# Kernel optimization log

Hardware: AMD Instinct MI355X
Metric: run time of the kernel (lower is better)

Reference implementation:

```python
import jax, jax.numpy as jnp
import numpy as np

B, N, R, D = 32, 256, 2048, 1024

def setup_inputs() -> dict:
    key = jax.random.key(0)
    ks = jax.random.split(key, 8)
    obj_vecs = jax.random.normal(ks[0], (B, N, D), dtype=jnp.float32)
    attr_vecs = jax.random.normal(ks[1], (B, N, D), dtype=jnp.float32)
    rela_vecs = jax.random.normal(ks[2], (B, R, D), dtype=jnp.float32)
    edges = jax.random.randint(ks[3], (B, R, 2), 0, N, dtype=jnp.int32)
    rela_masks = jnp.ones((B, R, 1), dtype=jnp.float32)
    # learned params: gnn_attr Linear(2D->D), gnn_rela Linear(3D->D)
    W_attr = jax.random.normal(ks[4], (D, 2 * D), dtype=jnp.float32) * 0.02
    b_attr = jnp.zeros((D,), dtype=jnp.float32)
    W_rela = jax.random.normal(ks[5], (D, 3 * D), dtype=jnp.float32) * 0.02
    b_rela = jnp.zeros((D,), dtype=jnp.float32)
    return {"obj_vecs": obj_vecs, "attr_vecs": attr_vecs, "rela_vecs": rela_vecs,
            "edges": edges, "rela_masks": rela_masks,
            "W_attr": W_attr, "b_attr": b_attr, "W_rela": W_rela, "b_rela": b_rela}

def reference(obj_vecs, attr_vecs, rela_vecs, edges, rela_masks,
              W_attr, b_attr, W_rela, b_rela):
    # gnn_attr: Linear(concat[obj,attr]) -> ReLU (-> dropout, identity in eval) + residual
    attr_in = jnp.concatenate([obj_vecs, attr_vecs], axis=-1)          # [B,N,2D]
    new_attr_vecs = jax.nn.relu(jnp.einsum('bnk,dk->bnd', attr_in, W_attr) + b_attr) + attr_vecs
    # gather subject/object node features per edge (per-batch indices)
    subj_idx = edges[:, :, 0:1]                                        # [B,R,1]
    obj_idx = edges[:, :, 1:2]
    subject_vecs = jnp.take_along_axis(obj_vecs, subj_idx, axis=1)     # [B,R,D]
    object_vecs = jnp.take_along_axis(obj_vecs, obj_idx, axis=1)       # [B,R,D]
    # rela_gnn_type == 0: triplet concat [subj | rela | obj]
    triplet = jnp.concatenate([subject_vecs, rela_vecs, object_vecs], axis=-1)  # [B,R,3D]
    new_rela_vecs = jax.nn.relu(jnp.einsum('brk,dk->brd', triplet, W_rela) + b_rela) + rela_vecs
    new_rela_vecs = new_rela_vecs * rela_masks                          # feat_2d_to_3d masking
    return (obj_vecs, new_attr_vecs, new_rela_vecs)
```

## Files before the change

### kernel.cpp

```cpp
#include <hip/hip_runtime.h>
#include <hip/hip_bf16.h>

constexpr int kB = 32;
constexpr int kN = 256;
constexpr int kR = 2048;
constexpr int kD = 1024;

typedef short bf16x8 __attribute__((ext_vector_type(8)));
typedef float f32x4 __attribute__((ext_vector_type(4)));
typedef unsigned short u16x8 __attribute__((ext_vector_type(8)));

__device__ __forceinline__ unsigned short f2bf(float f) {
  union { __hip_bfloat16 h; unsigned short u; } cv;
  cv.h = __float2bfloat16(f);
  return cv.u;
}
__device__ __forceinline__ float bf2f(unsigned short u) {
  union { unsigned int i; float f; } cv;
  cv.i = (unsigned int)u << 16;
  return cv.f;
}

__device__ __forceinline__ void gload_lds16(const void* g, void* l) {
  __builtin_amdgcn_global_load_lds(
      (const __attribute__((address_space(1))) unsigned int*)g,
      (__attribute__((address_space(3))) unsigned int*)l, 16, 0, 0);
}

#define FENCE asm volatile("" ::: "memory")
#define WAITV(n) asm volatile("s_waitcnt vmcnt(" #n ")" ::: "memory")

__global__ void cvt_all(const float* __restrict__ obj,
                        const float* __restrict__ attr,
                        const float* __restrict__ rela,
                        const float* __restrict__ wa,
                        const float* __restrict__ wr,
                        unsigned short* __restrict__ objb,
                        unsigned short* __restrict__ attrb,
                        unsigned short* __restrict__ relab,
                        unsigned short* __restrict__ wab,
                        unsigned short* __restrict__ wrb,
                        float* __restrict__ out0) {
  constexpr long n0 = (long)kB * kN * kD / 8;
  constexpr long c0 = n0;
  constexpr long c1 = c0 + n0;
  constexpr long c2 = c1 + (long)kB * kR * kD / 8;
  constexpr long c3 = c2 + (long)kD * 2 * kD / 8;
  constexpr long c4 = c3 + (long)kD * 3 * kD / 8;
  const long stride = (long)gridDim.x * blockDim.x;
  for (long i = (long)blockIdx.x * blockDim.x + threadIdx.x; i < c4;
       i += stride) {
    const float* s;
    unsigned short* d;
    long j;
    bool isobj = false;
    if (i < c0)      { s = obj;  d = objb;  j = i; isobj = true; }
    else if (i < c1) { s = attr; d = attrb; j = i - c0; }
    else if (i < c2) { s = rela; d = relab; j = i - c1; }
    else if (i < c3) { s = wa;   d = wab;   j = i - c2; }
    else             { s = wr;   d = wrb;   j = i - c3; }
    const float4 a = reinterpret_cast<const float4*>(s)[2 * j];
    const float4 b = reinterpret_cast<const float4*>(s)[2 * j + 1];
    if (isobj) {
      reinterpret_cast<float4*>(out0)[2 * j] = a;
      reinterpret_cast<float4*>(out0)[2 * j + 1] = b;
    }
    u16x8 v;
    v[0] = f2bf(a.x); v[1] = f2bf(a.y); v[2] = f2bf(a.z); v[3] = f2bf(a.w);
    v[4] = f2bf(b.x); v[5] = f2bf(b.y); v[6] = f2bf(b.z); v[7] = f2bf(b.w);
    reinterpret_cast<u16x8*>(d)[j] = v;
  }
}

template <int MODE, int NPANEL>
__device__ __forceinline__ void gemm_body(
    int bid, unsigned short* smem,
    const unsigned short* __restrict__ srcA0,
    const unsigned short* __restrict__ srcA1,
    const unsigned short* __restrict__ Wb, uint32_t koffB,
    const int* __restrict__ edges, const float* __restrict__ masks,
    const unsigned short* __restrict__ residB, const float* __restrict__ bias,
    const unsigned short* __restrict__ P1b,
    const unsigned short* __restrict__ P3b,
    float* __restrict__ outF, unsigned short* __restrict__ outP) {
  constexpr int K_TOT = (MODE == 0) ? 2048 : (MODE == 1) ? 3072 : 1024;
  constexpr int WST = (MODE == 0) ? 2048 : 3072;
  constexpr int T = K_TOT / 64;

  const int x = bid & 7;
  const int col0 = (x >> 1) * 256;
  const int panel = (x & 1) * (NPANEL / 2) + (bid >> 3);
  const int row0 = panel * 256;

  const int tid = threadIdx.x;
  const int w = tid >> 6;
  const int l = tid & 63;

  const int sw = (((l & 3) ^ ((l >> 3) & 3)) << 4);
  const char* pA0[2];
  const char* pA1[2];
  const char* pA2[2];
  const char* pB[2];
#pragma unroll
  for (int r = 0; r < 2; ++r) {
    const int rl = w * 32 + r * 16 + (l >> 2);
    const int m = row0 + rl;
    if constexpr (MODE == 1) {
      const int b = m >> 11;
      const int ri = m & 2047;
      const int2 e =
          *reinterpret_cast<const int2*>(&edges[((size_t)b * kR + ri) * 2]);
      pA0[r] = (const char*)(srcA0 + (size_t)(b * kN + e.x) * kD);
      pA1[r] = (const char*)(srcA1 + (size_t)m * kD);
      pA2[r] = (const char*)(srcA0 + (size_t)(b * kN + e.y) * kD);
    } else {
      pA0[r] = (const char*)(srcA0 + (size_t)m * kD);
      pA1[r] = (MODE == 0) ? (const char*)(srcA1 + (size_t)m * kD) : pA0[r];
      pA2[r] = pA0[r];
    }
    pB[r] = (const char*)Wb + (size_t)(col0 + rl) * WST * 2 + koffB;
  }

  const int wr = w >> 2;
  const int wc = w & 3;
  const int lrow = l & 15;
  const int lgrp = l >> 4;
  const int pgr = ((lgrp ^ ((lrow >> 1) & 3)) << 3);

  f32x4 acc[8][4] = {};
  bf16x8 AfX[4], AfY[4], Bf0[4], Bf1[4];

  auto issueA = [&](int tn, int h, int slot) {
    unsigned short* ra = smem + slot * 32768 + h * 8192;
    const int kb = tn * 64 + h * 32;
#pragma unroll
    for (int r = 0; r < 2; ++r) {
      const char* srcA;
      uint32_t ko;
      if constexpr (MODE == 1) {
        const int seg = kb >> 10;
        srcA = (seg == 1) ? pA1[r] : ((seg == 0) ? pA0[r] : pA2[r]);
        ko = (uint32_t)(kb & 1023) * 2;
      } else if constexpr (MODE == 0) {
        srcA = (kb < 1024) ? pA0[r] : pA1[r];
        ko = (uint32_t)(kb & 1023) * 2;
      } else {
        srcA = pA0[r];
        ko = (uint32_t)kb * 2;
      }
      gload_lds16(srcA + ko + sw, ra + (w * 2 + r) * 512);
    }
  };
  auto issueB = [&](int tn, int h, int slot) {
    unsigned short* rb = smem + slot * 32768 + 16384 + h * 8192;
    const uint32_t kb2 = (uint32_t)(tn * 64 + h * 32) * 2;
#pragma unroll
    for (int r = 0; r < 2; ++r)
      gload_lds16(pB[r] + kb2 + sw, rb + (w * 2 + r) * 512);
  };

#define RD_A4(SET, SLOT, KK, MOFF)                                         \
  _Pragma("unroll")                                                        \
  for (int mi = 0; mi < 4; ++mi)                                           \
    SET[mi] = *reinterpret_cast<const bf16x8*>(                            \
        &smem[(SLOT) * 32768 + (KK) * 8192 +                               \
              (wr * 128 + ((MOFF) + mi) * 16 + lrow) * 32 + pgr]);

#define RD_B4(SET, SLOT, KK)                                               \
  _Pragma("unroll")                                                        \
  for (int ni = 0; ni < 4; ++ni)                                           \
    SET[ni] = *reinterpret_cast<const bf16x8*>(                            \
        &smem[(SLOT) * 32768 + 16384 + (KK) * 8192 +                       \
              (wc * 64 + ni * 16 + lrow) * 32 + pgr]);

#define MFMA16(MOFF, ASET, BSET)                                           \
  __builtin_amdgcn_s_setprio(1);                                           \
  _Pragma("unroll")                                                        \
  for (int mi = 0; mi < 4; ++mi)                                           \
    _Pragma("unroll")                                                      \
    for (int ni = 0; ni < 4; ++ni)                                         \
      acc[(MOFF) + mi][ni] = __builtin_amdgcn_mfma_f32_16x16x32_bf16(      \
          ASET[mi], BSET[ni], acc[(MOFF) + mi][ni], 0, 0, 0);              \
  __builtin_amdgcn_s_setprio(0);

#define STILE(t, S)                                                        \
  {                                                                        \
    issueA((t) + 1, 0, (S) ^ 1);                                           \
    RD_A4(AfY, S, 0, 4);                                                   \
    MFMA16(0, AfX, Bf0);                                                   \
    issueB((t) + 1, 0, (S) ^ 1);                                           \
    WAITV(4);                                                              \
    __builtin_amdgcn_s_barrier();                                          \
    FENCE;                                                                 \
    RD_A4(AfX, S, 1, 0);                                                   \
    RD_B4(Bf1, S, 1);                                                      \
    MFMA16(4, AfY, Bf0);                                                   \
    issueA((t) + 1, 1, (S) ^ 1);                                           \
    RD_A4(AfY, S, 1, 4);                                                   \
    MFMA16(0, AfX, Bf1);                                                   \
    issueB((t) + 1, 1, (S) ^ 1);                                           \
    WAITV(4);                                                              \
    __builtin_amdgcn_s_barrier();                                          \
    FENCE;                                                                 \
    RD_A4(AfX, (S) ^ 1, 0, 0);                                             \
    RD_B4(Bf0, (S) ^ 1, 0);                                                \
    MFMA16(4, AfY, Bf1);                                                   \
  }

  issueA(0, 0, 0); issueB(0, 0, 0);
  issueA(0, 1, 0); issueB(0, 1, 0);
  WAITV(4);
  __builtin_amdgcn_s_barrier();
  FENCE;
  RD_A4(AfX, 0, 0, 0);
  RD_B4(Bf0, 0, 0);

#pragma unroll 1
  for (int it = 0; it < (T - 2) / 2; ++it) {
    STILE(2 * it, 0);
    STILE(2 * it + 1, 1);
  }
  STILE(T - 2, 0);

  {
    RD_A4(AfY, 1, 0, 4);
    MFMA16(0, AfX, Bf0);
    WAITV(0);
    __builtin_amdgcn_s_barrier();
    FENCE;
    RD_A4(AfX, 1, 1, 0);
    RD_B4(Bf1, 1, 1);
    MFMA16(4, AfY, Bf0);
    RD_A4(AfY, 1, 1, 4);
    MFMA16(0, AfX, Bf1);
    MFMA16(4, AfY, Bf1);
  }

#undef STILE
#undef MFMA16
#undef RD_B4
#undef RD_A4

  if constexpr (MODE == 2) {
#pragma unroll
    for (int mi = 0; mi < 8; ++mi) {
#pragma unroll
      for (int jj = 0; jj < 4; ++jj) {
        const int m = row0 + wr * 128 + mi * 16 + lgrp * 4 + jj;
        const size_t ro = (size_t)m * kD;
#pragma unroll
        for (int ni = 0; ni < 4; ++ni) {
          const int col = col0 + wc * 64 + ni * 16 + lrow;
          outP[ro + col] = f2bf(acc[mi][ni][jj]);
        }
      }
    }
    return;
  }

  float biasv[4];
#pragma unroll
  for (int ni = 0; ni < 4; ++ni)
    biasv[ni] = bias[col0 + wc * 64 + ni * 16 + lrow];

#pragma unroll
  for (int mi = 0; mi < 8; ++mi) {
#pragma unroll
    for (int jj = 0; jj < 4; ++jj) {
      const int m = row0 + wr * 128 + mi * 16 + lgrp * 4 + jj;
      const size_t ro = (size_t)m * kD;
      float mk = 1.0f;
      const unsigned short* p1row = nullptr;
      const unsigned short* p3row = nullptr;
      if constexpr (MODE == 1 || MODE == 3) mk = masks[m];
      if constexpr (MODE == 3) {
        const int b = m >> 11;
        const int2 e = reinterpret_cast<const int2*>(edges)[m];
        p1row = P1b + (size_t)(b * kN + e.x) * kD;
        p3row = P3b + (size_t)(b * kN + e.y) * kD;
      }
#pragma unroll
      for (int ni = 0; ni < 4; ++ni) {
        const int col = col0 + wc * 64 + ni * 16 + lrow;
        float v = acc[mi][ni][jj] + biasv[ni];
        if constexpr (MODE == 3) v += bf2f(p1row[col]) + bf2f(p3row[col]);
        v = fmaxf(v, 0.0f) + bf2f(residB[ro + col]);
        if constexpr (MODE == 1 || MODE == 3) v *= mk;
        __builtin_nontemporal_store(v, &outF[ro + col]);
      }
    }
  }
}

__global__ __launch_bounds__(512, 2) void gnn_small(
    const unsigned short* __restrict__ objb,
    const unsigned short* __restrict__ attrb,
    const unsigned short* __restrict__ wab,
    const unsigned short* __restrict__ wrb,
    const float* __restrict__ b_attr,
    float* __restrict__ out1, unsigned short* __restrict__ p1b,
    unsigned short* __restrict__ p3b) {
  extern __shared__ unsigned short smem[];
  const int bid = blockIdx.x;
  if (bid < 128) {
    gemm_body<0, 32>(bid, smem, objb, attrb, wab, 0, nullptr, nullptr, attrb,
                     b_attr, nullptr, nullptr, out1, nullptr);
  } else if (bid < 256) {
    gemm_body<2, 32>(bid - 128, smem, objb, nullptr, wrb, 0, nullptr, nullptr,
                     nullptr, nullptr, nullptr, nullptr, nullptr, p1b);
  } else {
    gemm_body<2, 32>(bid - 256, smem, objb, nullptr, wrb, 4096, nullptr,
                     nullptr, nullptr, nullptr, nullptr, nullptr, nullptr,
                     p3b);
  }
}

__global__ __launch_bounds__(512, 2) void gnn_rela(
    const unsigned short* __restrict__ relab,
    const unsigned short* __restrict__ wrb,
    const int* __restrict__ edges, const float* __restrict__ masks,
    const float* __restrict__ b_rela,
    const unsigned short* __restrict__ p1b,
    const unsigned short* __restrict__ p3b, float* __restrict__ out2) {
  extern __shared__ unsigned short smem[];
  gemm_body<3, 256>(blockIdx.x, smem, relab, nullptr, wrb, 2048, edges, masks,
                    relab, b_rela, p1b, p3b, out2, nullptr);
}

__global__ __launch_bounds__(512, 2) void gnn_fused(
    const unsigned short* __restrict__ objb,
    const unsigned short* __restrict__ attrb,
    const unsigned short* __restrict__ relab,
    const unsigned short* __restrict__ wab,
    const unsigned short* __restrict__ wrb,
    const int* __restrict__ edges, const float* __restrict__ masks,
    const float* __restrict__ b_attr, const float* __restrict__ b_rela,
    float* __restrict__ out1, float* __restrict__ out2) {
  extern __shared__ unsigned short smem[];
  const int bid = blockIdx.x;
  if (bid < 1024) {
    gemm_body<1, 256>(bid, smem, objb, relab, wrb, 0, edges, masks, relab,
                      b_rela, nullptr, nullptr, out2, nullptr);
  } else {
    gemm_body<0, 32>(bid - 1024, smem, objb, attrb, wab, 0, nullptr, nullptr,
                     attrb, b_attr, nullptr, nullptr, out1, nullptr);
  }
}

extern "C" void kernel_launch(void* const* d_in, const int* in_sizes, int n_in,
                              void* d_out, int out_size, void* d_ws,
                              size_t ws_size, hipStream_t stream) {
  (void)in_sizes; (void)n_in; (void)out_size;
  const float* obj = (const float*)d_in[0];
  const float* attr = (const float*)d_in[1];
  const float* rela = (const float*)d_in[2];
  const int* edges = (const int*)d_in[3];
  const float* masks = (const float*)d_in[4];
  const float* W_attr = (const float*)d_in[5];
  const float* b_attr = (const float*)d_in[6];
  const float* W_rela = (const float*)d_in[7];
  const float* b_rela = (const float*)d_in[8];

  float* out0 = (float*)d_out;
  float* out1 = out0 + (size_t)kB * kN * kD;
  float* out2 = out1 + (size_t)kB * kN * kD;

  constexpr size_t nObj = (size_t)kB * kN * kD;
  constexpr size_t nRela = (size_t)kB * kR * kD;
  constexpr size_t nWa = (size_t)kD * 2 * kD;
  constexpr size_t nWr = (size_t)kD * 3 * kD;

  unsigned short* objb = (unsigned short*)d_ws;
  unsigned short* attrb = objb + nObj;
  unsigned short* relab = attrb + nObj;
  unsigned short* wab = relab + nRela;
  unsigned short* wrb = wab + nWa;
  unsigned short* p1b = wrb + nWr;
  unsigned short* p3b = p1b + nObj;

  constexpr size_t WS_SPLIT = (nObj * 4 + nRela + nWa + nWr) * 2;

  cvt_all<<<2048, 256, 0, stream>>>(obj, attr, rela, W_attr, W_rela, objb,
                                    attrb, relab, wab, wrb, out0);

  constexpr int kSmem = 131072;
  if (ws_size >= WS_SPLIT) {
    hipFuncSetAttribute((const void*)gnn_small,
                        hipFuncAttributeMaxDynamicSharedMemorySize, kSmem);
    hipFuncSetAttribute((const void*)gnn_rela,
                        hipFuncAttributeMaxDynamicSharedMemorySize, kSmem);
    gnn_small<<<384, 512, kSmem, stream>>>(objb, attrb, wab, wrb, b_attr,
                                           out1, p1b, p3b);
    gnn_rela<<<1024, 512, kSmem, stream>>>(relab, wrb, edges, masks, b_rela,
                                           p1b, p3b, out2);
  } else {
    hipFuncSetAttribute((const void*)gnn_fused,
                        hipFuncAttributeMaxDynamicSharedMemorySize, kSmem);
    gnn_fused<<<1152, 512, kSmem, stream>>>(objb, attrb, relab, wab, wrb,
                                            edges, masks, b_attr, b_rela,
                                            out1, out2);
  }
}
```

Baseline: 422.3 us.

## Overlap rela bf16 conversion with small GEMMs via extra converter blocks

The rela fp32-to-bf16 conversion, the largest part of the conversion work, moves out of the upfront conversion kernel. It now runs in 1664 extra blocks appended to the small-GEMM launch, so it overlaps with the attr and P1/P3 projection GEMMs. This is meant to hide the memory-bound conversion behind compute-bound GEMM work. The trade-off is that converter blocks use the same 128KB shared-memory launch config, which limits occupancy for those blocks, and the block scheduler may not interleave them well with the GEMM blocks.

```diff
diff --git a/kernel.cpp b/kernel.cpp
--- a/kernel.cpp
+++ b/kernel.cpp
@@ -29,6 +29,52 @@
 
 #define FENCE asm volatile("" ::: "memory")
 #define WAITV(n) asm volatile("s_waitcnt vmcnt(" #n ")" ::: "memory")
+
+__device__ __forceinline__ void cvt8(const float* __restrict__ s,
+                                     unsigned short* __restrict__ d, long j) {
+  const float4 a = reinterpret_cast<const float4*>(s)[2 * j];
+  const float4 b = reinterpret_cast<const float4*>(s)[2 * j + 1];
+  u16x8 v;
+  v[0] = f2bf(a.x); v[1] = f2bf(a.y); v[2] = f2bf(a.z); v[3] = f2bf(a.w);
+  v[4] = f2bf(b.x); v[5] = f2bf(b.y); v[6] = f2bf(b.z); v[7] = f2bf(b.w);
+  reinterpret_cast<u16x8*>(d)[j] = v;
+}
+
+__global__ void cvt_front(const float* __restrict__ obj,
+                          const float* __restrict__ attr,
+                          const float* __restrict__ wa,
+                          const float* __restrict__ wr,
+                          unsigned short* __restrict__ objb,
+                          unsigned short* __restrict__ attrb,
+                          unsigned short* __restrict__ wab,
+                          unsigned short* __restrict__ wrb,
+                          float* __restrict__ out0) {
+  constexpr long n0 = (long)kB * kN * kD / 8;
+  constexpr long c0 = n0;
+  constexpr long c1 = c0 + n0;
+  constexpr long c2 = c1 + (long)kD * 2 * kD / 8;
+  constexpr long c3 = c2 + (long)kD * 3 * kD / 8;
+  const long stride = (long)gridDim.x * blockDim.x;
+  for (long i = (long)blockIdx.x * blockDim.x + threadIdx.x; i < c3;
+       i += stride) {
+    if (i < c0) {
+      const float4 a = reinterpret_cast<const float4*>(obj)[2 * i];
+      const float4 b = reinterpret_cast<const float4*>(obj)[2 * i + 1];
+      reinterpret_cast<float4*>(out0)[2 * i] = a;
+      reinterpret_cast<float4*>(out0)[2 * i + 1] = b;
+      u16x8 v;
+      v[0] = f2bf(a.x); v[1] = f2bf(a.y); v[2] = f2bf(a.z); v[3] = f2bf(a.w);
+      v[4] = f2bf(b.x); v[5] = f2bf(b.y); v[6] = f2bf(b.z); v[7] = f2bf(b.w);
+      reinterpret_cast<u16x8*>(objb)[i] = v;
+    } else if (i < c1) {
+      cvt8(attr, attrb, i - c0);
+    } else if (i < c2) {
+      cvt8(wa, wab, i - c1);
+    } else {
+      cvt8(wr, wrb, i - c2);
+    }
+  }
+}
 
 __global__ void cvt_all(const float* __restrict__ obj,
                         const float* __restrict__ attr,
@@ -50,25 +96,19 @@
   const long stride = (long)gridDim.x * blockDim.x;
   for (long i = (long)blockIdx.x * blockDim.x + threadIdx.x; i < c4;
        i += stride) {
-    const float* s;
-    unsigned short* d;
-    long j;
-    bool isobj = false;
-    if (i < c0)      { s = obj;  d = objb;  j = i; isobj = true; }
-    else if (i < c1) { s = attr; d = attrb; j = i - c0; }
-    else if (i < c2) { s = rela; d = relab; j = i - c1; }
-    else if (i < c3) { s = wa;   d = wab;   j = i - c2; }
-    else             { s = wr;   d = wrb;   j = i - c3; }
-    const float4 a = reinterpret_cast<const float4*>(s)[2 * j];
-    const float4 b = reinterpret_cast<const float4*>(s)[2 * j + 1];
-    if (isobj) {
-      reinterpret_cast<float4*>(out0)[2 * j] = a;
-      reinterpret_cast<float4*>(out0)[2 * j + 1] = b;
-    }
-    u16x8 v;
-    v[0] = f2bf(a.x); v[1] = f2bf(a.y); v[2] = f2bf(a.z); v[3] = f2bf(a.w);
-    v[4] = f2bf(b.x); v[5] = f2bf(b.y); v[6] = f2bf(b.z); v[7] = f2bf(b.w);
-    reinterpret_cast<u16x8*>(d)[j] = v;
+    if (i < c0) {
+      const float4 a = reinterpret_cast<const float4*>(obj)[2 * i];
+      const float4 b = reinterpret_cast<const float4*>(obj)[2 * i + 1];
+      reinterpret_cast<float4*>(out0)[2 * i] = a;
+      reinterpret_cast<float4*>(out0)[2 * i + 1] = b;
+      u16x8 v;
+      v[0] = f2bf(a.x); v[1] = f2bf(a.y); v[2] = f2bf(a.z); v[3] = f2bf(a.w);
+      v[4] = f2bf(b.x); v[5] = f2bf(b.y); v[6] = f2bf(b.z); v[7] = f2bf(b.w);
+      reinterpret_cast<u16x8*>(objb)[i] = v;
+    } else if (i < c1) cvt8(attr, attrb, i - c0);
+    else if (i < c2) cvt8(rela, relab, i - c1);
+    else if (i < c3) cvt8(wa, wab, i - c2);
+    else cvt8(wr, wrb, i - c3);
   }
 }
 
@@ -292,14 +332,14 @@
   }
 }
 
-__global__ __launch_bounds__(512, 2) void gnn_small(
+__global__ __launch_bounds__(512, 2) void gnn_small_cvt(
     const unsigned short* __restrict__ objb,
     const unsigned short* __restrict__ attrb,
     const unsigned short* __restrict__ wab,
     const unsigned short* __restrict__ wrb,
-    const float* __restrict__ b_attr,
-    float* __restrict__ out1, unsigned short* __restrict__ p1b,
-    unsigned short* __restrict__ p3b) {
+    const float* __restrict__ b_attr, float* __restrict__ out1,
+    unsigned short* __restrict__ p1b, unsigned short* __restrict__ p3b,
+    const float* __restrict__ rela, unsigned short* __restrict__ relab) {
   extern __shared__ unsigned short smem[];
   const int bid = blockIdx.x;
   if (bid < 128) {
@@ -308,10 +348,15 @@
   } else if (bid < 256) {
     gemm_body<2, 32>(bid - 128, smem, objb, nullptr, wrb, 0, nullptr, nullptr,
                      nullptr, nullptr, nullptr, nullptr, nullptr, p1b);
-  } else {
+  } else if (bid < 384) {
     gemm_body<2, 32>(bid - 256, smem, objb, nullptr, wrb, 4096, nullptr,
                      nullptr, nullptr, nullptr, nullptr, nullptr, nullptr,
                      p3b);
+  } else {
+    constexpr long n8 = (long)kB * kR * kD / 8;
+    const long nth = (long)(2048 - 384) * 512;
+    for (long i = (long)(bid - 384) * 512 + threadIdx.x; i < n8; i += nth)
+      cvt8(rela, relab, i);
   }
 }
 
@@ -379,21 +424,22 @@
   unsigned short* p3b = p1b + nObj;
 
   constexpr size_t WS_SPLIT = (nObj * 4 + nRela + nWa + nWr) * 2;
-
-  cvt_all<<<2048, 256, 0, stream>>>(obj, attr, rela, W_attr, W_rela, objb,
-                                    attrb, relab, wab, wrb, out0);
-
   constexpr int kSmem = 131072;
+
   if (ws_size >= WS_SPLIT) {
-    hipFuncSetAttribute((const void*)gnn_small,
+    cvt_front<<<2048, 256, 0, stream>>>(obj, attr, W_attr, W_rela, objb,
+                                        attrb, wab, wrb, out0);
+    hipFuncSetAttribute((const void*)gnn_small_cvt,
                         hipFuncAttributeMaxDynamicSharedMemorySize, kSmem);
     hipFuncSetAttribute((const void*)gnn_rela,
                         hipFuncAttributeMaxDynamicSharedMemorySize, kSmem);
-    gnn_small<<<384, 512, kSmem, stream>>>(objb, attrb, wab, wrb, b_attr,
-                                           out1, p1b, p3b);
+    gnn_small_cvt<<<2048, 512, kSmem, stream>>>(objb, attrb, wab, wrb, b_attr,
+                                                out1, p1b, p3b, rela, relab);
     gnn_rela<<<1024, 512, kSmem, stream>>>(relab, wrb, edges, masks, b_rela,
                                            p1b, p3b, out2);
   } else {
+    cvt_all<<<2048, 256, 0, stream>>>(obj, attr, rela, W_attr, W_rela, objb,
+                                      attrb, relab, wab, wrb, out0);
     hipFuncSetAttribute((const void*)gnn_fused,
                         hipFuncAttributeMaxDynamicSharedMemorySize, kSmem);
     gnn_fused<<<1152, 512, kSmem, stream>>>(objb, attrb, relab, wab, wrb,
```

Measured after the change: 422.9 us, median of 2. About the same (+0.1%).
